# Kernel tuning notes

Measured on AMD Instinct MI355X. Metric: run time of the kernel, lower is better.

Reference implementation:

```python
import jax, jax.numpy as jnp
import numpy as np

M, P, B, TLEN = 512, 256, 128, 1024

def setup_inputs() -> dict:
    key = jax.random.key(0)
    k1, k2, k3, k4, k5, k6 = jax.random.split(key, 6)
    d_t = jax.random.normal(k1, (1, B, P), dtype=jnp.float32)
    s_t = jax.random.normal(k2, (1, B, P), dtype=jnp.float32)
    H = jax.random.normal(k3, (B, TLEN, M), dtype=jnp.float32)
    # torch.nn.Linear weights: shape [out_features, in_features]
    W_d = jax.random.normal(k4, (M, 2 * P), dtype=jnp.float32) / np.sqrt(2 * P)
    U_d = jax.random.normal(k5, (M, M), dtype=jnp.float32) / np.sqrt(M)
    v_d = jax.random.normal(k6, (1, M), dtype=jnp.float32) / np.sqrt(M)
    return {"d_t": d_t, "s_t": s_t, "H": H, "T": TLEN, "W_d": W_d, "U_d": U_d, "v_d": v_d}

def reference(d_t, s_t, H, T, W_d, U_d, v_d):
    # query: cat([d_t, s_t], dim=2) -> [1, B, 2p]; permute(1,0,2) -> [B, 1, 2p]
    query = jnp.concatenate([d_t, s_t], axis=2).transpose(1, 0, 2)  # [B, 1, 2p]
    # W_d(query) broadcast over T instead of materializing the repeat (same math)
    wq = jnp.einsum('boc,mc->bom', query, W_d)          # [B, 1, m]
    uh = jnp.einsum('btm,nm->btn', H, U_d)              # [B, T, m]
    beta = jnp.tanh(wq + uh)                            # [B, T, m]
    score = jnp.einsum('btm,om->bto', beta, v_d)        # [B, T, 1]
    score = score.transpose(0, 2, 1)                    # [B, 1, T]
    return jax.nn.softmax(score, axis=2)
```

## Files before the change

kernel.cpp:

```cpp
#include <hip/hip_runtime.h>
#include <hip/hip_bf16.h>
#include <stdint.h>

#define NB   128
#define NT   1024
#define NM   512
#define NP   256

typedef __attribute__((ext_vector_type(8))) short bf16x8;
typedef __attribute__((ext_vector_type(4))) float f32x4;

__device__ __forceinline__ uint32_t bfpair(float a, float b) {
    uint32_t ua = __float_as_uint(a) + 0x8000u;
    uint32_t ub = __float_as_uint(b) + 0x8000u;
    return __builtin_amdgcn_perm(ub, ua, 0x07060302u);
}

__device__ __forceinline__ float fast_tanh(float x) {
    float e = __expf(2.0f * x);
    return 1.0f - 2.0f * __builtin_amdgcn_rcpf(e + 1.0f);
}

__global__ void prep_kernel(const float* __restrict__ U, unsigned short* __restrict__ Ub,
                            const float* __restrict__ d_t, const float* __restrict__ s_t,
                            const float* __restrict__ W, float* __restrict__ wq) {
    if (blockIdx.x < 256) {
        int idx = blockIdx.x * 256 + threadIdx.x;
        float4 u = reinterpret_cast<const float4*>(U)[idx];
        reinterpret_cast<uint2*>(Ub)[idx] = make_uint2(bfpair(u.x, u.y), bfpair(u.z, u.w));
    } else {
        int g = (blockIdx.x - 256) * 512 + threadIdx.x * 2;
        int b = g >> 9;
        const float* dt = d_t + (size_t)b * NP;
        const float* st = s_t + (size_t)b * NP;
        #pragma unroll
        for (int e = 0; e < 2; ++e) {
            int n = (g + e) & 511;
            const float* Wn = W + (size_t)n * 512;
            float s = 0.f;
            #pragma unroll 4
            for (int c = 0; c < NP; c += 4) {
                float4 w0 = *reinterpret_cast<const float4*>(Wn + c);
                float4 q0 = *reinterpret_cast<const float4*>(dt + c);
                s += w0.x * q0.x + w0.y * q0.y + w0.z * q0.z + w0.w * q0.w;
                float4 w1 = *reinterpret_cast<const float4*>(Wn + NP + c);
                float4 q1 = *reinterpret_cast<const float4*>(st + c);
                s += w1.x * q1.x + w1.y * q1.y + w1.z * q1.z + w1.w * q1.w;
            }
            wq[g + e] = s;
        }
    }
}

__global__ __launch_bounds__(256, 2)
void score_kernel(const float* __restrict__ H, const unsigned short* __restrict__ Ub,
                  const float* __restrict__ wq, const float* __restrict__ v_d,
                  float* __restrict__ out) {
    __shared__ unsigned short As[2][64 * 40];
    __shared__ float s_score[64];

    const int tid  = threadIdx.x;
    const int b    = blockIdx.y;
    const int t0   = blockIdx.x * 64;
    const int lane = tid & 63;
    const int w    = tid >> 6;
    const int lr   = lane & 15;
    const int lq   = lane >> 4;

    if (tid < 64) s_score[tid] = 0.f;

    const int r0 = tid >> 3;
    const int r1 = (tid + 256) >> 3;
    const int c4 = (tid & 7) * 4;
    const float* HbA = H + ((size_t)b * NT + t0) * NM;

    const unsigned short* pB = Ub + ((size_t)(w * 128 + lr)) * NM + lq * 8;

    f32x4 acc[4][8];
    #pragma unroll
    for (int i = 0; i < 4; ++i)
        #pragma unroll
        for (int j = 0; j < 8; ++j)
            acc[i][j] = (f32x4){0.f, 0.f, 0.f, 0.f};

    bf16x8 bq[2][8];

    {
        float4 f0 = *reinterpret_cast<const float4*>(HbA + (size_t)r0 * NM + c4);
        float4 f1 = *reinterpret_cast<const float4*>(HbA + (size_t)r1 * NM + c4);
        #pragma unroll
        for (int j = 0; j < 8; ++j)
            bq[0][j] = *reinterpret_cast<const bf16x8*>(pB + (size_t)j * 16 * NM);
        *reinterpret_cast<uint2*>(&As[0][r0 * 40 + c4]) = make_uint2(bfpair(f0.x, f0.y), bfpair(f0.z, f0.w));
        *reinterpret_cast<uint2*>(&As[0][r1 * 40 + c4]) = make_uint2(bfpair(f1.x, f1.y), bfpair(f1.z, f1.w));
    }
    __syncthreads();

    #pragma unroll
    for (int kk = 0; kk < 16; ++kk) {
        const int cur = kk & 1;
        const int nxt = cur ^ 1;

        float4 f0, f1;
        if (kk < 15) {
            const int k0 = (kk + 1) * 32;
            f0 = *reinterpret_cast<const float4*>(HbA + (size_t)r0 * NM + k0 + c4);
            f1 = *reinterpret_cast<const float4*>(HbA + (size_t)r1 * NM + k0 + c4);
            #pragma unroll
            for (int j = 0; j < 8; ++j)
                bq[nxt][j] = *reinterpret_cast<const bf16x8*>(pB + (size_t)j * 16 * NM + k0);
        }

        bf16x8 a[4];
        #pragma unroll
        for (int i = 0; i < 4; ++i)
            a[i] = *reinterpret_cast<const bf16x8*>(&As[cur][(i * 16 + lr) * 40 + lq * 8]);

        #pragma unroll
        for (int i = 0; i < 4; ++i)
            #pragma unroll
            for (int j = 0; j < 8; ++j)
                acc[i][j] = __builtin_amdgcn_mfma_f32_16x16x32_bf16(a[i], bq[cur][j], acc[i][j], 0, 0, 0);

        if (kk < 15) {
            *reinterpret_cast<uint2*>(&As[nxt][r0 * 40 + c4]) = make_uint2(bfpair(f0.x, f0.y), bfpair(f0.z, f0.w));
            *reinterpret_cast<uint2*>(&As[nxt][r1 * 40 + c4]) = make_uint2(bfpair(f1.x, f1.y), bfpair(f1.z, f1.w));
            __syncthreads();
        }
    }

    const float* wqb = wq + (size_t)b * NM;
    float vv[8], wv[8];
    #pragma unroll
    for (int j = 0; j < 8; ++j) {
        int n = w * 128 + j * 16 + lr;
        vv[j] = v_d[n];
        wv[j] = wqb[n];
    }
    #pragma unroll
    for (int i = 0; i < 4; ++i) {
        #pragma unroll
        for (int r = 0; r < 4; ++r) {
            float s = 0.f;
            #pragma unroll
            for (int j = 0; j < 8; ++j)
                s += vv[j] * fast_tanh(wv[j] + acc[i][j][r]);
            #pragma unroll
            for (int off = 1; off < 16; off <<= 1)
                s += __shfl_xor(s, off, 64);
            if (lr == 0) atomicAdd(&s_score[i * 16 + lq * 4 + r], s);
        }
    }
    __syncthreads();
    if (tid < 64) out[(size_t)b * NT + t0 + tid] = s_score[tid];
}

__global__ void softmax_kernel(float* __restrict__ out) {
    const int b   = blockIdx.x;
    const int tid = threadIdx.x;
    float* p = out + (size_t)b * NT;
    float4 v = reinterpret_cast<float4*>(p)[tid];
    float m = fmaxf(fmaxf(v.x, v.y), fmaxf(v.z, v.w));
    #pragma unroll
    for (int off = 32; off >= 1; off >>= 1)
        m = fmaxf(m, __shfl_xor(m, off, 64));
    __shared__ float red[8];
    const int wv = tid >> 6;
    if ((tid & 63) == 0) red[wv] = m;
    __syncthreads();
    m = fmaxf(fmaxf(red[0], red[1]), fmaxf(red[2], red[3]));
    float e0 = __expf(v.x - m), e1 = __expf(v.y - m);
    float e2 = __expf(v.z - m), e3 = __expf(v.w - m);
    float s = e0 + e1 + e2 + e3;
    #pragma unroll
    for (int off = 32; off >= 1; off >>= 1)
        s += __shfl_xor(s, off, 64);
    if ((tid & 63) == 0) red[4 + wv] = s;
    __syncthreads();
    s = red[4] + red[5] + red[6] + red[7];
    float inv = 1.f / s;
    float4 o;
    o.x = e0 * inv; o.y = e1 * inv; o.z = e2 * inv; o.w = e3 * inv;
    reinterpret_cast<float4*>(p)[tid] = o;
}

extern "C" void kernel_launch(void* const* d_in, const int* in_sizes, int n_in,
                              void* d_out, int out_size, void* d_ws, size_t ws_size,
                              hipStream_t stream) {
    const float* d_t = (const float*)d_in[0];
    const float* s_t = (const float*)d_in[1];
    const float* H   = (const float*)d_in[2];
    const float* W_d = (const float*)d_in[4];
    const float* U_d = (const float*)d_in[5];
    const float* v_d = (const float*)d_in[6];
    float* out = (float*)d_out;

    unsigned short* Ub = (unsigned short*)d_ws;
    float* wq = (float*)((char*)d_ws + 512 * 1024);

    prep_kernel<<<384, 256, 0, stream>>>(U_d, Ub, d_t, s_t, W_d, wq);
    score_kernel<<<dim3(NT / 64, NB), 256, 0, stream>>>(H, Ub, wq, v_d, out);
    softmax_kernel<<<NB, 256, 0, stream>>>(out);
}
```

Baseline: 508.2 us.

## Retile score GEMM to 128x256 tiles with async global-to-LDS loads and N-split atomics

Each score block now covers 128 time rows and half of the M columns, where before it covered 64 rows and all of M. H and U tiles are copied straight into swizzled LDS with global_load_lds, and the fp32 H tile is converted to bf16 after it is read from LDS. The two N-halves combine their partial scores through global atomicAdd into an output that prep_kernel now zeroes. The aim is to cut per-block U reloads and register-staged global loads and to overlap copies with MFMA, at the cost of twice as much LDS traffic for the fp32 A tile, global atomics, and a launch order that interleaves the two halves of each tile.

```diff
diff --git a/kernel.cpp b/kernel.cpp
--- a/kernel.cpp
+++ b/kernel.cpp
@@ -9,6 +9,7 @@
 
 typedef __attribute__((ext_vector_type(8))) short bf16x8;
 typedef __attribute__((ext_vector_type(4))) float f32x4;
+typedef unsigned int u32;
 
 __device__ __forceinline__ uint32_t bfpair(float a, float b) {
     uint32_t ua = __float_as_uint(a) + 0x8000u;
@@ -16,20 +17,37 @@
     return __builtin_amdgcn_perm(ub, ua, 0x07060302u);
 }
 
+__device__ __forceinline__ bf16x8 pack8(float4 lo, float4 hi) {
+    union { bf16x8 v; uint32_t u[4]; } r;
+    r.u[0] = bfpair(lo.x, lo.y);
+    r.u[1] = bfpair(lo.z, lo.w);
+    r.u[2] = bfpair(hi.x, hi.y);
+    r.u[3] = bfpair(hi.z, hi.w);
+    return r.v;
+}
+
 __device__ __forceinline__ float fast_tanh(float x) {
     float e = __expf(2.0f * x);
     return 1.0f - 2.0f * __builtin_amdgcn_rcpf(e + 1.0f);
 }
 
+typedef const __attribute__((address_space(1))) u32* gas_t;
+typedef __attribute__((address_space(3))) u32* las_t;
+__device__ __forceinline__ void dma16(const void* g, void* l) {
+    __builtin_amdgcn_global_load_lds((gas_t)g, (las_t)l, 16, 0, 0);
+}
+
 __global__ void prep_kernel(const float* __restrict__ U, unsigned short* __restrict__ Ub,
                             const float* __restrict__ d_t, const float* __restrict__ s_t,
-                            const float* __restrict__ W, float* __restrict__ wq) {
-    if (blockIdx.x < 256) {
-        int idx = blockIdx.x * 256 + threadIdx.x;
+                            const float* __restrict__ W, float* __restrict__ wq,
+                            float* __restrict__ out) {
+    const int bx = blockIdx.x;
+    if (bx < 256) {
+        int idx = bx * 256 + threadIdx.x;
         float4 u = reinterpret_cast<const float4*>(U)[idx];
         reinterpret_cast<uint2*>(Ub)[idx] = make_uint2(bfpair(u.x, u.y), bfpair(u.z, u.w));
-    } else {
-        int g = (blockIdx.x - 256) * 512 + threadIdx.x * 2;
+    } else if (bx < 384) {
+        int g = (bx - 256) * 512 + threadIdx.x * 2;
         int b = g >> 9;
         const float* dt = d_t + (size_t)b * NP;
         const float* st = s_t + (size_t)b * NP;
@@ -49,6 +67,9 @@
             }
             wq[g + e] = s;
         }
+    } else {
+        int idx = (bx - 384) * 256 + threadIdx.x;
+        reinterpret_cast<float4*>(out)[idx] = make_float4(0.f, 0.f, 0.f, 0.f);
     }
 }
 
@@ -56,25 +77,39 @@
 void score_kernel(const float* __restrict__ H, const unsigned short* __restrict__ Ub,
                   const float* __restrict__ wq, const float* __restrict__ v_d,
                   float* __restrict__ out) {
-    __shared__ unsigned short As[2][64 * 40];
-    __shared__ float s_score[64];
+    __shared__ float          As[2][128 * 32];
+    __shared__ unsigned short Bs[2][256 * 32];
+    __shared__ float s_score[128];
 
     const int tid  = threadIdx.x;
-    const int b    = blockIdx.y;
-    const int t0   = blockIdx.x * 64;
+    const int id   = blockIdx.x;
+    const int tile = (id >> 4) * 8 + (id & 7);
+    const int nh   = (id >> 3) & 1;
+    const int tt   = tile & 7;
+    const int b    = tile >> 3;
+
     const int lane = tid & 63;
     const int w    = tid >> 6;
     const int lr   = lane & 15;
     const int lq   = lane >> 4;
-
-    if (tid < 64) s_score[tid] = 0.f;
-
-    const int r0 = tid >> 3;
-    const int r1 = (tid + 256) >> 3;
-    const int c4 = (tid & 7) * 4;
-    const float* HbA = H + ((size_t)b * NT + t0) * NM;
-
-    const unsigned short* pB = Ub + ((size_t)(w * 128 + lr)) * NM + lq * 8;
+    const int tw   = w >> 1;
+    const int nw   = w & 1;
+
+    if (tid < 128) s_score[tid] = 0.f;
+
+    const float* gA[4];
+    const unsigned short* gB[4];
+    unsigned lL[4];
+    #pragma unroll
+    for (int q = 0; q < 4; ++q) {
+        int rA = w * 32 + q * 8 + (lane >> 3);
+        int cA = (lane & 7) ^ (rA & 7);
+        gA[q] = H + ((size_t)(b * NT + tt * 128 + rA)) * NM + cA * 4;
+        int rB = w * 64 + q * 16 + (lane >> 2);
+        int cB = (lane & 3) ^ ((rB >> 1) & 3);
+        gB[q] = Ub + ((size_t)(nh * 256 + rB)) * NM + cB * 8;
+        lL[q] = (unsigned)((w * 4 + q) * 1024 + lane * 16);
+    }
 
     f32x4 acc[4][8];
     #pragma unroll
@@ -83,57 +118,53 @@
         for (int j = 0; j < 8; ++j)
             acc[i][j] = (f32x4){0.f, 0.f, 0.f, 0.f};
 
-    bf16x8 bq[2][8];
-
-    {
-        float4 f0 = *reinterpret_cast<const float4*>(HbA + (size_t)r0 * NM + c4);
-        float4 f1 = *reinterpret_cast<const float4*>(HbA + (size_t)r1 * NM + c4);
-        #pragma unroll
-        for (int j = 0; j < 8; ++j)
-            bq[0][j] = *reinterpret_cast<const bf16x8*>(pB + (size_t)j * 16 * NM);
-        *reinterpret_cast<uint2*>(&As[0][r0 * 40 + c4]) = make_uint2(bfpair(f0.x, f0.y), bfpair(f0.z, f0.w));
-        *reinterpret_cast<uint2*>(&As[0][r1 * 40 + c4]) = make_uint2(bfpair(f1.x, f1.y), bfpair(f1.z, f1.w));
-    }
-    __syncthreads();
+    #pragma unroll
+    for (int q = 0; q < 4; ++q) dma16(gA[q], (char*)As[0] + lL[q]);
+    #pragma unroll
+    for (int q = 0; q < 4; ++q) dma16(gB[q], (char*)Bs[0] + lL[q]);
 
     #pragma unroll
     for (int kk = 0; kk < 16; ++kk) {
         const int cur = kk & 1;
         const int nxt = cur ^ 1;
-
-        float4 f0, f1;
+        __syncthreads();
         if (kk < 15) {
-            const int k0 = (kk + 1) * 32;
-            f0 = *reinterpret_cast<const float4*>(HbA + (size_t)r0 * NM + k0 + c4);
-            f1 = *reinterpret_cast<const float4*>(HbA + (size_t)r1 * NM + k0 + c4);
+            #pragma unroll
+            for (int q = 0; q < 4; ++q) { gA[q] += 32; dma16(gA[q], (char*)As[nxt] + lL[q]); }
+            #pragma unroll
+            for (int q = 0; q < 4; ++q) { gB[q] += 32; dma16(gB[q], (char*)Bs[nxt] + lL[q]); }
+        }
+
+        bf16x8 a[4];
+        #pragma unroll
+        for (int i = 0; i < 4; ++i) {
+            int t_loc = tw * 64 + i * 16 + lr;
+            int s = t_loc & 7;
+            const char* base = (const char*)As[cur] + t_loc * 128;
+            float4 lo = *reinterpret_cast<const float4*>(base + (((2 * lq)     ^ s) * 16));
+            float4 hi = *reinterpret_cast<const float4*>(base + (((2 * lq + 1) ^ s) * 16));
+            a[i] = pack8(lo, hi);
+        }
+        bf16x8 bb[8];
+        #pragma unroll
+        for (int j = 0; j < 8; ++j) {
+            int n_loc = nw * 128 + j * 16 + lr;
+            int slot = lq ^ ((n_loc >> 1) & 3);
+            bb[j] = *reinterpret_cast<const bf16x8*>((const char*)Bs[cur] + n_loc * 64 + slot * 16);
+        }
+
+        #pragma unroll
+        for (int i = 0; i < 4; ++i)
             #pragma unroll
             for (int j = 0; j < 8; ++j)
-                bq[nxt][j] = *reinterpret_cast<const bf16x8*>(pB + (size_t)j * 16 * NM + k0);
-        }
-
-        bf16x8 a[4];
-        #pragma unroll
-        for (int i = 0; i < 4; ++i)
-            a[i] = *reinterpret_cast<const bf16x8*>(&As[cur][(i * 16 + lr) * 40 + lq * 8]);
-
-        #pragma unroll
-        for (int i = 0; i < 4; ++i)
-            #pragma unroll
-            for (int j = 0; j < 8; ++j)
-                acc[i][j] = __builtin_amdgcn_mfma_f32_16x16x32_bf16(a[i], bq[cur][j], acc[i][j], 0, 0, 0);
-
-        if (kk < 15) {
-            *reinterpret_cast<uint2*>(&As[nxt][r0 * 40 + c4]) = make_uint2(bfpair(f0.x, f0.y), bfpair(f0.z, f0.w));
-            *reinterpret_cast<uint2*>(&As[nxt][r1 * 40 + c4]) = make_uint2(bfpair(f1.x, f1.y), bfpair(f1.z, f1.w));
-            __syncthreads();
-        }
+                acc[i][j] = __builtin_amdgcn_mfma_f32_16x16x32_bf16(a[i], bb[j], acc[i][j], 0, 0, 0);
     }
 
     const float* wqb = wq + (size_t)b * NM;
     float vv[8], wv[8];
     #pragma unroll
     for (int j = 0; j < 8; ++j) {
-        int n = w * 128 + j * 16 + lr;
+        int n = nh * 256 + nw * 128 + j * 16 + lr;
         vv[j] = v_d[n];
         wv[j] = wqb[n];
     }
@@ -148,11 +179,11 @@
             #pragma unroll
             for (int off = 1; off < 16; off <<= 1)
                 s += __shfl_xor(s, off, 64);
-            if (lr == 0) atomicAdd(&s_score[i * 16 + lq * 4 + r], s);
+            if (lr == 0) atomicAdd(&s_score[tw * 64 + i * 16 + lq * 4 + r], s);
         }
     }
     __syncthreads();
-    if (tid < 64) out[(size_t)b * NT + t0 + tid] = s_score[tid];
+    if (tid < 128) atomicAdd(&out[(size_t)b * NT + tt * 128 + tid], s_score[tid]);
 }
 
 __global__ void softmax_kernel(float* __restrict__ out) {
@@ -198,7 +229,7 @@
     unsigned short* Ub = (unsigned short*)d_ws;
     float* wq = (float*)((char*)d_ws + 512 * 1024);
 
-    prep_kernel<<<384, 256, 0, stream>>>(U_d, Ub, d_t, s_t, W_d, wq);
-    score_kernel<<<dim3(NT / 64, NB), 256, 0, stream>>>(H, Ub, wq, v_d, out);
+    prep_kernel<<<512, 256, 0, stream>>>(U_d, Ub, d_t, s_t, W_d, wq, out);
+    score_kernel<<<2048, 256, 0, stream>>>(H, Ub, wq, v_d, out);
     softmax_kernel<<<NB, 256, 0, stream>>>(out);
 }
```

After: 467.0 us. 1.09x faster.
